# Kernel optimization log

Measured on AMD Instinct MI355X. Metric: run time of the kernel, lower is better.

Reference implementation:

```python
import jax, jax.numpy as jnp
import numpy as np

N = 50000   # num nodes
E = 600000  # num edges per signed adjacency
D = 128     # feature dim
K = 10      # num_diff_layers
C = 0.15    # restart probability


def setup_inputs() -> dict:
    key = jax.random.key(0)
    ks = jax.random.split(key, 8)
    rows_p = jax.random.randint(ks[0], (E,), 0, N, dtype=jnp.int32)
    cols_p = jax.random.randint(ks[1], (E,), 0, N, dtype=jnp.int32)
    vals_p = jax.random.uniform(ks[2], (E,), dtype=jnp.float32)
    rows_m = jax.random.randint(ks[3], (E,), 0, N, dtype=jnp.int32)
    cols_m = jax.random.randint(ks[4], (E,), 0, N, dtype=jnp.int32)
    vals_m = jax.random.uniform(ks[5], (E,), dtype=jnp.float32)
    X = jax.random.normal(ks[6], (N, D), dtype=jnp.float32)
    # torch code draws old_M ~ Uniform(-1, 1) at forward time; we expose it as input
    M0 = jax.random.uniform(ks[7], (N, D), dtype=jnp.float32, minval=-1.0, maxval=1.0)
    return {"rows_p": rows_p, "cols_p": cols_p, "vals_p": vals_p,
            "rows_m": rows_m, "cols_m": cols_m, "vals_m": vals_m,
            "X": X, "M0": M0}


def _spmm(rows, cols, vals, dense):
    # COO sparse [N,N] @ dense [N,D]: gather columns, scale, scatter-add to rows
    return jax.ops.segment_sum(vals[:, None] * dense[cols], rows,
                               num_segments=dense.shape[0])


def reference(rows_p, cols_p, vals_p, rows_m, cols_m, vals_m, X, M0):
    tilda_X = C * X  # restart term
    P, M = X, M0
    for _ in range(K):
        new_P = _spmm(rows_p, cols_p, vals_p, P) + _spmm(rows_m, cols_m, vals_m, M) + tilda_X
        new_M = _spmm(rows_m, cols_m, vals_m, P) + _spmm(rows_p, cols_p, vals_p, M)
        P, M = new_P, new_M
    return (P, M)
```

## Files before the change

kernel.cpp:

```cpp
#include <hip/hip_runtime.h>
#include <math.h>


#define TB 256

__device__ __forceinline__ unsigned pack_bf16(float a, float b) {
    unsigned ua = __float_as_uint(a), ub = __float_as_uint(b);
    ua += 0x7fffu + ((ua >> 16) & 1u);
    ub += 0x7fffu + ((ub >> 16) & 1u);
    return (ua >> 16) | (ub & 0xffff0000u);
}

__device__ __forceinline__ float2 unpack_bf16(unsigned w) {
    float2 r;
    r.x = __uint_as_float(w << 16);
    r.y = __uint_as_float(w & 0xffff0000u);
    return r;
}

__global__ void zero_int_kernel(int* __restrict__ p, int n) {
    int i = blockIdx.x * blockDim.x + threadIdx.x;
    if (i < n) p[i] = 0;
}

__global__ void copy_int_kernel(const int* __restrict__ src, int* __restrict__ dst, int n) {
    int i = blockIdx.x * blockDim.x + threadIdx.x;
    if (i < n) dst[i] = src[i];
}

__global__ void hist_kernel(const int* __restrict__ rows, int E, int* __restrict__ cnt) {
    int e = blockIdx.x * blockDim.x + threadIdx.x;
    if (e < E) atomicAdd(&cnt[rows[e]], 1);
}

__global__ void scanA_kernel(const int* __restrict__ cnt, int* __restrict__ bsum, int n) {
    __shared__ int wsum[16];
    int tid = threadIdx.x, lane = tid & 63, wid = tid >> 6;
    int i = blockIdx.x * 1024 + tid;
    int x = (i < n) ? cnt[i] : 0;
#pragma unroll
    for (int o = 1; o < 64; o <<= 1) { int y = __shfl_up(x, o); if (lane >= o) x += y; }
    if (lane == 63) wsum[wid] = x;
    __syncthreads();
    if (tid == 0) {
        int s = 0;
#pragma unroll
        for (int w = 0; w < 16; ++w) s += wsum[w];
        bsum[blockIdx.x] = s;
    }
}

__global__ void scanB_kernel(int* __restrict__ bsum, int nb) {
    __shared__ int wsum[16];
    int tid = threadIdx.x, lane = tid & 63, wid = tid >> 6;
    int x = (tid < nb) ? bsum[tid] : 0;
    int incl = x;
#pragma unroll
    for (int o = 1; o < 64; o <<= 1) { int y = __shfl_up(incl, o); if (lane >= o) incl += y; }
    if (lane == 63) wsum[wid] = incl;
    __syncthreads();
    if (wid == 0) {
        int s = (lane < 16) ? wsum[lane] : 0;
#pragma unroll
        for (int o = 1; o < 16; o <<= 1) { int y = __shfl_up(s, o); if (lane >= o) s += y; }
        if (lane < 16) wsum[lane] = s;
    }
    __syncthreads();
    int base = (wid > 0) ? wsum[wid - 1] : 0;
    if (tid < nb) bsum[tid] = base + incl - x;
}

__global__ void scanC_kernel(const int* __restrict__ cnt, const int* __restrict__ bsum,
                             int* __restrict__ off, int n) {
    __shared__ int wsum[16];
    int tid = threadIdx.x, lane = tid & 63, wid = tid >> 6;
    int i = blockIdx.x * 1024 + tid;
    int x = (i < n) ? cnt[i] : 0;
    int incl = x;
#pragma unroll
    for (int o = 1; o < 64; o <<= 1) { int y = __shfl_up(incl, o); if (lane >= o) incl += y; }
    if (lane == 63) wsum[wid] = incl;
    __syncthreads();
    if (wid == 0) {
        int s = (lane < 16) ? wsum[lane] : 0;
#pragma unroll
        for (int o = 1; o < 16; o <<= 1) { int y = __shfl_up(s, o); if (lane >= o) s += y; }
        if (lane < 16) wsum[lane] = s;
    }
    __syncthreads();
    int base = bsum[blockIdx.x] + ((wid > 0) ? wsum[wid - 1] : 0);
    if (i < n) {
        off[i] = base + incl - x;
        if (i == n - 1) off[n] = base + incl;
    }
}

__global__ void fill_kernel(const int* __restrict__ rows, const int* __restrict__ cols,
                            const float* __restrict__ vals, int E, float sgn,
                            int* __restrict__ cur, int* __restrict__ ccol,
                            float* __restrict__ cval) {
    int e = blockIdx.x * blockDim.x + threadIdx.x;
    if (e < E) {
        int r = rows[e];
        int p = atomicAdd(&cur[r], 1);
        ccol[p] = cols[e];
        cval[p] = sgn * vals[e];
    }
}

__global__ void init_kernel(const float* __restrict__ X, const float* __restrict__ M0,
                            unsigned* __restrict__ Sb, unsigned* __restrict__ Db,
                            unsigned* __restrict__ tXb, int n) {
    int i = blockIdx.x * blockDim.x + threadIdx.x;
    if (i < n) {
        float2 x = ((const float2*)X)[i];
        float2 m = ((const float2*)M0)[i];
        Sb[i]  = pack_bf16(x.x + m.x, x.y + m.y);
        Db[i]  = pack_bf16(x.x - m.x, x.y - m.y);
        tXb[i] = pack_bf16(0.15f * x.x, 0.15f * x.y);
    }
}

__global__ void final_kernel(const unsigned* __restrict__ Sb, const unsigned* __restrict__ Db,
                             float* __restrict__ P, float* __restrict__ M, int n) {
    int i = blockIdx.x * blockDim.x + threadIdx.x;
    if (i < n) {
        float2 s = unpack_bf16(Sb[i]);
        float2 d = unpack_bf16(Db[i]);
        ((float2*)P)[i] = make_float2(0.5f * (s.x + d.x), 0.5f * (s.y + d.y));
        ((float2*)M)[i] = make_float2(0.5f * (s.x - d.x), 0.5f * (s.y - d.y));
    }
}

__global__ __launch_bounds__(TB) void layer_kernel(
    const int* __restrict__ off, const int* __restrict__ col,
    const float* __restrict__ val,
    const unsigned* __restrict__ Sin, const unsigned* __restrict__ Din,
    unsigned* __restrict__ Sout, unsigned* __restrict__ Dout,
    const unsigned* __restrict__ tXb, int N) {
    int row = blockIdx.x * (TB / 64) + (threadIdx.x >> 6);
    if (row >= N) return;
    int lane = threadIdx.x & 63;
    int sys = blockIdx.y;
    const unsigned* __restrict__ In  = sys ? Din : Sin;
    unsigned* __restrict__       Out = sys ? Dout : Sout;

    int ridx = row * 64 + lane;
    float2 t = unpack_bf16(tXb[ridx]);
    float ax = t.x, ay = t.y;

    int b = off[row], e = off[row + 1];
    int j = b;
    for (; j + 4 <= e; j += 4) {
        int c0 = col[j], c1 = col[j + 1], c2 = col[j + 2], c3 = col[j + 3];
        float v0 = val[j], v1 = val[j + 1], v2 = val[j + 2], v3 = val[j + 3];
        if (!sys) { v0 = fabsf(v0); v1 = fabsf(v1); v2 = fabsf(v2); v3 = fabsf(v3); }
        unsigned w0 = In[c0 * 64 + lane];
        unsigned w1 = In[c1 * 64 + lane];
        unsigned w2 = In[c2 * 64 + lane];
        unsigned w3 = In[c3 * 64 + lane];
        float2 g0 = unpack_bf16(w0), g1 = unpack_bf16(w1);
        float2 g2 = unpack_bf16(w2), g3 = unpack_bf16(w3);
        ax += v0 * g0.x + v1 * g1.x + v2 * g2.x + v3 * g3.x;
        ay += v0 * g0.y + v1 * g1.y + v2 * g2.y + v3 * g3.y;
    }
    for (; j < e; ++j) {
        int c = col[j];
        float v = val[j];
        if (!sys) v = fabsf(v);
        float2 g = unpack_bf16(In[c * 64 + lane]);
        ax += v * g.x;
        ay += v * g.y;
    }
    Out[ridx] = pack_bf16(ax, ay);
}

extern "C" void kernel_launch(void* const* d_in, const int* in_sizes, int n_in,
                              void* d_out, int out_size, void* d_ws, size_t ws_size,
                              hipStream_t stream) {
    const int*   rows_p = (const int*)d_in[0];
    const int*   cols_p = (const int*)d_in[1];
    const float* vals_p = (const float*)d_in[2];
    const int*   rows_m = (const int*)d_in[3];
    const int*   cols_m = (const int*)d_in[4];
    const float* vals_m = (const float*)d_in[5];
    const float* X      = (const float*)d_in[6];
    const float* M0     = (const float*)d_in[7];

    const int E = in_sizes[0];
    const int D = 128;
    const int N = in_sizes[6] / D;
    const int K = 10;
    const int E2 = 2 * E;
    const size_t ND = (size_t)N * D;
    const int NP = (int)(ND / 2);

    float* outP = (float*)d_out;
    float* outM = outP + ND;

    char* ws = (char*)d_ws;
    size_t o = 0;
    auto alloc = [&](size_t b) -> void* {
        void* p = ws + o;
        o += (b + 255) & ~(size_t)255;
        return p;
    };
    unsigned* SbA = (unsigned*)alloc((size_t)NP * 4);
    unsigned* DbA = (unsigned*)alloc((size_t)NP * 4);
    unsigned* SbB = (unsigned*)alloc((size_t)NP * 4);
    unsigned* DbB = (unsigned*)alloc((size_t)NP * 4);
    unsigned* tXb = (unsigned*)alloc((size_t)NP * 4);
    int*   cnt  = (int*)alloc((size_t)N * sizeof(int));
    int*   off  = (int*)alloc((size_t)(N + 1) * sizeof(int));
    int*   cur  = (int*)alloc((size_t)N * sizeof(int));
    int*   bsum = (int*)alloc(1024 * sizeof(int));
    int*   col  = (int*)alloc((size_t)E2 * sizeof(int));
    float* val  = (float*)alloc((size_t)E2 * sizeof(float));

    int gN  = (N + TB - 1) / TB;
    int gE  = (E + TB - 1) / TB;
    int gNP = (NP + TB - 1) / TB;
    int nb  = (N + 1023) / 1024;

    zero_int_kernel<<<gN, TB, 0, stream>>>(cnt, N);
    hist_kernel<<<gE, TB, 0, stream>>>(rows_p, E, cnt);
    hist_kernel<<<gE, TB, 0, stream>>>(rows_m, E, cnt);
    scanA_kernel<<<nb, 1024, 0, stream>>>(cnt, bsum, N);
    scanB_kernel<<<1, 1024, 0, stream>>>(bsum, nb);
    scanC_kernel<<<nb, 1024, 0, stream>>>(cnt, bsum, off, N);
    copy_int_kernel<<<gN, TB, 0, stream>>>(off, cur, N);
    fill_kernel<<<gE, TB, 0, stream>>>(rows_p, cols_p, vals_p, E,  1.0f, cur, col, val);
    fill_kernel<<<gE, TB, 0, stream>>>(rows_m, cols_m, vals_m, E, -1.0f, cur, col, val);

    init_kernel<<<gNP, TB, 0, stream>>>(X, M0, SbA, DbA, tXb, NP);

    dim3 gL((N + (TB / 64) - 1) / (TB / 64), 2);
    unsigned *Si = SbA, *Di = DbA, *So = SbB, *Do = DbB;
    for (int k = 0; k < K; ++k) {
        layer_kernel<<<gL, TB, 0, stream>>>(off, col, val, Si, Di, So, Do, tXb, N);
        unsigned* t;
        t = Si; Si = So; So = t;
        t = Di; Di = Do; Do = t;
    }

    final_kernel<<<gNP, TB, 0, stream>>>(Si, Di, outP, outM, NP);
}
```

Before: 1.190 ms.

## Pack CSR edges as int2, fuse setup kernels, interleave S/D blocks, unroll gather by 8

Column index and value are packed into one int2 per CSR edge, so the layer kernel issues one 8-byte load per edge instead of two separate streams. The setup path fuses the two histogram and two fill launches into one each and writes the cursor array inside the scan, which removes the copy kernel. The layer grid becomes 1D and interleaves S and D system blocks for neighbouring rows so both systems read the same edge lists close together in time. The gather loop is unrolled to 8 to put more independent loads in flight, at some cost in registers.

```diff
diff --git a/kernel.cpp b/kernel.cpp
--- a/kernel.cpp
+++ b/kernel.cpp
@@ -23,14 +23,13 @@
     if (i < n) p[i] = 0;
 }
 
-__global__ void copy_int_kernel(const int* __restrict__ src, int* __restrict__ dst, int n) {
-    int i = blockIdx.x * blockDim.x + threadIdx.x;
-    if (i < n) dst[i] = src[i];
-}
-
-__global__ void hist_kernel(const int* __restrict__ rows, int E, int* __restrict__ cnt) {
+__global__ void hist2_kernel(const int* __restrict__ rows_p, const int* __restrict__ rows_m,
+                             int E, int* __restrict__ cnt) {
     int e = blockIdx.x * blockDim.x + threadIdx.x;
-    if (e < E) atomicAdd(&cnt[rows[e]], 1);
+    if (e < 2 * E) {
+        int r = (e < E) ? rows_p[e] : rows_m[e - E];
+        atomicAdd(&cnt[r], 1);
+    }
 }
 
 __global__ void scanA_kernel(const int* __restrict__ cnt, int* __restrict__ bsum, int n) {
@@ -71,7 +70,7 @@
 }
 
 __global__ void scanC_kernel(const int* __restrict__ cnt, const int* __restrict__ bsum,
-                             int* __restrict__ off, int n) {
+                             int* __restrict__ off, int* __restrict__ cur, int n) {
     __shared__ int wsum[16];
     int tid = threadIdx.x, lane = tid & 63, wid = tid >> 6;
     int i = blockIdx.x * 1024 + tid;
@@ -90,21 +89,25 @@
     __syncthreads();
     int base = bsum[blockIdx.x] + ((wid > 0) ? wsum[wid - 1] : 0);
     if (i < n) {
-        off[i] = base + incl - x;
+        int ex = base + incl - x;
+        off[i] = ex;
+        cur[i] = ex;
         if (i == n - 1) off[n] = base + incl;
     }
 }
 
-__global__ void fill_kernel(const int* __restrict__ rows, const int* __restrict__ cols,
-                            const float* __restrict__ vals, int E, float sgn,
-                            int* __restrict__ cur, int* __restrict__ ccol,
-                            float* __restrict__ cval) {
+__global__ void fill2_kernel(const int* __restrict__ rows_p, const int* __restrict__ cols_p,
+                             const float* __restrict__ vals_p,
+                             const int* __restrict__ rows_m, const int* __restrict__ cols_m,
+                             const float* __restrict__ vals_m, int E,
+                             int* __restrict__ cur, int2* __restrict__ edge) {
     int e = blockIdx.x * blockDim.x + threadIdx.x;
-    if (e < E) {
-        int r = rows[e];
+    if (e < 2 * E) {
+        int r, c; float v;
+        if (e < E) { r = rows_p[e]; c = cols_p[e]; v =  vals_p[e]; }
+        else       { r = rows_m[e - E]; c = cols_m[e - E]; v = -vals_m[e - E]; }
         int p = atomicAdd(&cur[r], 1);
-        ccol[p] = cols[e];
-        cval[p] = sgn * vals[e];
+        edge[p] = make_int2(c, __float_as_int(v));
     }
 }
 
@@ -133,15 +136,17 @@
 }
 
 __global__ __launch_bounds__(TB) void layer_kernel(
-    const int* __restrict__ off, const int* __restrict__ col,
-    const float* __restrict__ val,
+    const int* __restrict__ off, const int2* __restrict__ edge,
     const unsigned* __restrict__ Sin, const unsigned* __restrict__ Din,
     unsigned* __restrict__ Sout, unsigned* __restrict__ Dout,
     const unsigned* __restrict__ tXb, int N) {
-    int row = blockIdx.x * (TB / 64) + (threadIdx.x >> 6);
+    int b = blockIdx.x;
+    int slot = b & 7;
+    int sys = slot >> 2;
+    int r4 = (b >> 3) * 4 + (slot & 3);
+    int row = r4 * 4 + (threadIdx.x >> 6);
     if (row >= N) return;
     int lane = threadIdx.x & 63;
-    int sys = blockIdx.y;
     const unsigned* __restrict__ In  = sys ? Din : Sin;
     unsigned* __restrict__       Out = sys ? Dout : Sout;
 
@@ -149,26 +154,41 @@
     float2 t = unpack_bf16(tXb[ridx]);
     float ax = t.x, ay = t.y;
 
-    int b = off[row], e = off[row + 1];
-    int j = b;
-    for (; j + 4 <= e; j += 4) {
-        int c0 = col[j], c1 = col[j + 1], c2 = col[j + 2], c3 = col[j + 3];
-        float v0 = val[j], v1 = val[j + 1], v2 = val[j + 2], v3 = val[j + 3];
-        if (!sys) { v0 = fabsf(v0); v1 = fabsf(v1); v2 = fabsf(v2); v3 = fabsf(v3); }
-        unsigned w0 = In[c0 * 64 + lane];
-        unsigned w1 = In[c1 * 64 + lane];
-        unsigned w2 = In[c2 * 64 + lane];
-        unsigned w3 = In[c3 * 64 + lane];
+    int bg = off[row], e = off[row + 1];
+    int j = bg;
+    for (; j + 8 <= e; j += 8) {
+        int2 e0 = edge[j],     e1 = edge[j + 1], e2 = edge[j + 2], e3 = edge[j + 3];
+        int2 e4 = edge[j + 4], e5 = edge[j + 5], e6 = edge[j + 6], e7 = edge[j + 7];
+        unsigned w0 = In[e0.x * 64 + lane];
+        unsigned w1 = In[e1.x * 64 + lane];
+        unsigned w2 = In[e2.x * 64 + lane];
+        unsigned w3 = In[e3.x * 64 + lane];
+        unsigned w4 = In[e4.x * 64 + lane];
+        unsigned w5 = In[e5.x * 64 + lane];
+        unsigned w6 = In[e6.x * 64 + lane];
+        unsigned w7 = In[e7.x * 64 + lane];
+        float v0 = __int_as_float(e0.y), v1 = __int_as_float(e1.y);
+        float v2 = __int_as_float(e2.y), v3 = __int_as_float(e3.y);
+        float v4 = __int_as_float(e4.y), v5 = __int_as_float(e5.y);
+        float v6 = __int_as_float(e6.y), v7 = __int_as_float(e7.y);
+        if (!sys) {
+            v0 = fabsf(v0); v1 = fabsf(v1); v2 = fabsf(v2); v3 = fabsf(v3);
+            v4 = fabsf(v4); v5 = fabsf(v5); v6 = fabsf(v6); v7 = fabsf(v7);
+        }
         float2 g0 = unpack_bf16(w0), g1 = unpack_bf16(w1);
         float2 g2 = unpack_bf16(w2), g3 = unpack_bf16(w3);
-        ax += v0 * g0.x + v1 * g1.x + v2 * g2.x + v3 * g3.x;
-        ay += v0 * g0.y + v1 * g1.y + v2 * g2.y + v3 * g3.y;
+        float2 g4 = unpack_bf16(w4), g5 = unpack_bf16(w5);
+        float2 g6 = unpack_bf16(w6), g7 = unpack_bf16(w7);
+        ax += v0 * g0.x + v1 * g1.x + v2 * g2.x + v3 * g3.x
+            + v4 * g4.x + v5 * g5.x + v6 * g6.x + v7 * g7.x;
+        ay += v0 * g0.y + v1 * g1.y + v2 * g2.y + v3 * g3.y
+            + v4 * g4.y + v5 * g5.y + v6 * g6.y + v7 * g7.y;
     }
     for (; j < e; ++j) {
-        int c = col[j];
-        float v = val[j];
+        int2 ed = edge[j];
+        float v = __int_as_float(ed.y);
         if (!sys) v = fabsf(v);
-        float2 g = unpack_bf16(In[c * 64 + lane]);
+        float2 g = unpack_bf16(In[ed.x * 64 + lane]);
         ax += v * g.x;
         ay += v * g.y;
     }
@@ -205,39 +225,37 @@
         o += (b + 255) & ~(size_t)255;
         return p;
     };
-    unsigned* SbA = (unsigned*)alloc((size_t)NP * 4);
-    unsigned* DbA = (unsigned*)alloc((size_t)NP * 4);
-    unsigned* SbB = (unsigned*)alloc((size_t)NP * 4);
-    unsigned* DbB = (unsigned*)alloc((size_t)NP * 4);
-    unsigned* tXb = (unsigned*)alloc((size_t)NP * 4);
-    int*   cnt  = (int*)alloc((size_t)N * sizeof(int));
-    int*   off  = (int*)alloc((size_t)(N + 1) * sizeof(int));
-    int*   cur  = (int*)alloc((size_t)N * sizeof(int));
-    int*   bsum = (int*)alloc(1024 * sizeof(int));
-    int*   col  = (int*)alloc((size_t)E2 * sizeof(int));
-    float* val  = (float*)alloc((size_t)E2 * sizeof(float));
+    unsigned* SbA  = (unsigned*)alloc((size_t)NP * 4);
+    unsigned* DbA  = (unsigned*)alloc((size_t)NP * 4);
+    unsigned* SbB  = (unsigned*)alloc((size_t)NP * 4);
+    unsigned* DbB  = (unsigned*)alloc((size_t)NP * 4);
+    unsigned* tXb  = (unsigned*)alloc((size_t)NP * 4);
+    int*      cnt  = (int*)alloc((size_t)N * sizeof(int));
+    int*      off  = (int*)alloc((size_t)(N + 1) * sizeof(int));
+    int*      cur  = (int*)alloc((size_t)N * sizeof(int));
+    int*      bsum = (int*)alloc(1024 * sizeof(int));
+    int2*     edge = (int2*)alloc((size_t)E2 * sizeof(int2));
 
     int gN  = (N + TB - 1) / TB;
-    int gE  = (E + TB - 1) / TB;
+    int gE2 = (E2 + TB - 1) / TB;
     int gNP = (NP + TB - 1) / TB;
     int nb  = (N + 1023) / 1024;
 
     zero_int_kernel<<<gN, TB, 0, stream>>>(cnt, N);
-    hist_kernel<<<gE, TB, 0, stream>>>(rows_p, E, cnt);
-    hist_kernel<<<gE, TB, 0, stream>>>(rows_m, E, cnt);
+    hist2_kernel<<<gE2, TB, 0, stream>>>(rows_p, rows_m, E, cnt);
     scanA_kernel<<<nb, 1024, 0, stream>>>(cnt, bsum, N);
     scanB_kernel<<<1, 1024, 0, stream>>>(bsum, nb);
-    scanC_kernel<<<nb, 1024, 0, stream>>>(cnt, bsum, off, N);
-    copy_int_kernel<<<gN, TB, 0, stream>>>(off, cur, N);
-    fill_kernel<<<gE, TB, 0, stream>>>(rows_p, cols_p, vals_p, E,  1.0f, cur, col, val);
-    fill_kernel<<<gE, TB, 0, stream>>>(rows_m, cols_m, vals_m, E, -1.0f, cur, col, val);
+    scanC_kernel<<<nb, 1024, 0, stream>>>(cnt, bsum, off, cur, N);
+    fill2_kernel<<<gE2, TB, 0, stream>>>(rows_p, cols_p, vals_p,
+                                         rows_m, cols_m, vals_m, E, cur, edge);
 
     init_kernel<<<gNP, TB, 0, stream>>>(X, M0, SbA, DbA, tXb, NP);
 
-    dim3 gL((N + (TB / 64) - 1) / (TB / 64), 2);
+    int blocks_per_sys = (N + 3) / 4;
+    int gridx = ((blocks_per_sys + 3) / 4) * 8;
     unsigned *Si = SbA, *Di = DbA, *So = SbB, *Do = DbB;
     for (int k = 0; k < K; ++k) {
-        layer_kernel<<<gL, TB, 0, stream>>>(off, col, val, Si, Di, So, Do, tXb, N);
+        layer_kernel<<<gridx, TB, 0, stream>>>(off, edge, Si, Di, So, Do, tXb, N);
         unsigned* t;
         t = Si; Si = So; So = t;
         t = Di; Di = Do; Do = t;
```

After: 1.158 ms. 1.03x faster.
